# Kernel tuning notes

Measured on AMD Instinct MI355X. Metric: run time of the kernel, lower is better.

The kernel has to match this reference:

```python
import jax, jax.numpy as jnp
import numpy as np

MAX_WORDS = 256  # = batch['labels'].shape[1]


def _align(hidden, word_ids, max_words):
    """Batched segment-mean: (B,S,D) subtoken states -> (B,max_words,D) word states.
    Equivalent to align_subtokens_to_words applied per sample (word_ids all valid)."""
    B, S, D = hidden.shape
    seg = (word_ids.astype(jnp.int32) + jnp.arange(B, dtype=jnp.int32)[:, None] * max_words).reshape(-1)
    sums = jax.ops.segment_sum(hidden.reshape(-1, D), seg, num_segments=B * max_words)
    cnts = jax.ops.segment_sum(jnp.ones((B * S,), hidden.dtype), seg, num_segments=B * max_words)
    out = jnp.where(cnts[:, None] > 0, sums / jnp.maximum(cnts, 1.0)[:, None], 0.0)
    return out.reshape(B, max_words, D)


def setup_inputs() -> dict:
    key = jax.random.key(0)
    ks = jax.random.split(key, 8)
    B, S, D, W = 64, 512, 768, MAX_WORDS
    h_hing_sub = jax.random.normal(ks[0], (B, S, D), dtype=jnp.float32)
    h_rob_sub = jax.random.normal(ks[1], (B, S, D), dtype=jnp.float32)
    hing_word_ids = jnp.sort(jax.random.randint(ks[2], (B, S), 0, W), axis=-1).astype(jnp.int32)
    rob_word_ids = jnp.sort(jax.random.randint(ks[3], (B, S), 0, W), axis=-1).astype(jnp.int32)
    num_words = jax.random.randint(ks[4], (B,), 1, W).astype(jnp.int32)
    router_w1 = jax.random.normal(ks[5], (2 * D, 256), dtype=jnp.float32) * (1.0 / np.sqrt(2 * D))
    router_b1 = jnp.zeros((256,), jnp.float32)
    router_w2 = jax.random.normal(ks[6], (256, 1), dtype=jnp.float32) * (1.0 / 16.0)
    router_b2 = jnp.zeros((1,), jnp.float32)
    head_w = jax.random.normal(ks[7], (D, 7), dtype=jnp.float32) * (1.0 / np.sqrt(D))
    head_b = jnp.zeros((7,), jnp.float32)
    return {
        'h_hing_sub': h_hing_sub, 'h_rob_sub': h_rob_sub,
        'hing_word_ids': hing_word_ids, 'rob_word_ids': rob_word_ids,
        'num_words': num_words,
        'router_w1': router_w1, 'router_b1': router_b1,
        'router_w2': router_w2, 'router_b2': router_b2,
        'head_w': head_w, 'head_b': head_b,
    }


def reference(h_hing_sub, h_rob_sub, hing_word_ids, rob_word_ids, num_words,
              router_w1, router_b1, router_w2, router_b2, head_w, head_b):
    W = MAX_WORDS
    # scatter-mean subtokens -> words (the dominant custom-kernel op)
    h_hing = _align(h_hing_sub, hing_word_ids, W)   # (B, W, 768)
    h_rob = _align(h_rob_sub, rob_word_ids, W)      # (B, W, 768)
    # token-level MLP router on concatenated word states (router_input='both')
    router_in = jnp.concatenate([h_hing, h_rob], axis=-1)             # (B, W, 1536)
    hdn = jax.nn.relu(jnp.einsum('bwd,dh->bwh', router_in, router_w1) + router_b1)
    alpha = jax.nn.sigmoid(jnp.einsum('bwh,ho->bwo', hdn, router_w2) + router_b2)  # (B, W, 1)
    blended = alpha * h_hing + (1.0 - alpha) * h_rob                  # (B, W, 768)
    logits = jnp.einsum('bwd,dl->bwl', blended, head_w) + head_b      # (B, W, num_labels)
    l2_disagreement = jnp.linalg.norm(h_hing - h_rob, axis=-1)        # (B, W)
    return logits, alpha.squeeze(-1), l2_disagreement
```

## Files before the change

### kernel.cpp

```cpp
#include <hip/hip_runtime.h>
#include <hip/hip_bf16.h>
#include <math.h>

#define BATCH 64
#define SEQ   512
#define DIM   768
#define NW    256
#define NT    (BATCH * NW)
#define KDIM  1536
#define HID   256
#define NL    7

#define BM  32
#define BK  64
#define BKP 72
#define NKT (KDIM / BK)

typedef __bf16 bf16_t;
typedef bf16_t bf16x4 __attribute__((ext_vector_type(4)));
typedef bf16_t bf16x8 __attribute__((ext_vector_type(8)));
typedef float  f32x4  __attribute__((ext_vector_type(4)));

__global__ __launch_bounds__(256) void prep_kernel(
    const float* __restrict__ w1, bf16_t* __restrict__ w1t,
    const int* __restrict__ idh, const int* __restrict__ idr,
    int* __restrict__ starts)
{
    if (blockIdx.x < 192) {
        int kc = blockIdx.x >> 3;
        int kg = blockIdx.x & 7;
        int n  = threadIdx.x;
        bf16x8 v;
        #pragma unroll
        for (int j = 0; j < 8; j++)
            v[j] = (bf16_t)w1[(size_t)(kc * 64 + kg * 8 + j) * HID + n];
        *(bf16x8*)(w1t + (size_t)kc * (HID * BK) + n * BK + kg * 8) = v;
    } else {
        int blk = blockIdx.x - 192;
        int t = blk >> 6;
        int b = blk & 63;
        const int* ids = (t ? idr : idh) + b * SEQ;
        int w = threadIdx.x;
        int lo = 0, hi = SEQ;
        while (lo < hi) {
            int m = (lo + hi) >> 1;
            if (ids[m] < w) lo = m + 1; else hi = m;
        }
        int* row = starts + blk * 257;
        row[w] = lo;
        if (w == 0) row[256] = SEQ;
    }
}

__global__ __launch_bounds__(256) void align_kernel(
    const float* __restrict__ hh, const float* __restrict__ hr,
    const int* __restrict__ starts, bf16_t* __restrict__ X)
{
    int bid  = blockIdx.x;
    int swz  = (bid & 7) * 3072 + (bid >> 3);

    int idx  = swz * 256 + threadIdx.x;
    int rest = idx / 192;
    int c    = idx - rest * 192;
    rest     = __builtin_amdgcn_readfirstlane(rest);
    int w    = rest & 255;
    int t    = (rest >> 8) & 1;
    int b    = rest >> 9;

    const int* st = starts + (t * 64 + b) * 257;
    int lo = st[w];
    int hi = st[w + 1];

    const f32x4* src = (const f32x4*)((t ? hr : hh) + (size_t)b * SEQ * DIM);
    bf16_t*      dst = X + (size_t)b * NW * KDIM + (size_t)w * KDIM
                         + t * DIM + c * 4;

    bf16x4 o = {};
    int n = hi - lo;
    if (n > 0) {
        f32x4 acc = src[(size_t)lo * 192 + c];
        for (int s = lo + 1; s < hi; s++) {
            f32x4 v = src[(size_t)s * 192 + c];
            acc[0] += v[0]; acc[1] += v[1];
            acc[2] += v[2]; acc[3] += v[3];
        }
        float inv = 1.0f / (float)n;
        o[0] = (bf16_t)(acc[0] * inv);
        o[1] = (bf16_t)(acc[1] * inv);
        o[2] = (bf16_t)(acc[2] * inv);
        o[3] = (bf16_t)(acc[3] * inv);
    }
    *(bf16x4*)dst = o;
}

__global__ __launch_bounds__(256) void gemm_alpha_kernel(
    const bf16_t* __restrict__ X, const bf16_t* __restrict__ w1t,
    const float* __restrict__ b1, const float* __restrict__ w2,
    const float* __restrict__ b2, float* __restrict__ out)
{
    __shared__ __align__(16) bf16_t Xs[BM][BKP];
    __shared__ __align__(16) bf16_t Ws[HID][BKP];
    __shared__ float alpha_acc[BM];

    int tid   = threadIdx.x;
    int lane  = tid & 63;
    int wv    = tid >> 6;
    int row16 = lane & 15;
    int quad  = lane >> 4;
    int tok0  = blockIdx.x * BM;

    f32x4 acc[2][4];
    #pragma unroll
    for (int mi = 0; mi < 2; mi++)
        #pragma unroll
        for (int ni = 0; ni < 4; ni++)
            acc[mi][ni] = (f32x4){0.f, 0.f, 0.f, 0.f};

    int xr = tid >> 3;
    int xc = tid & 7;

    for (int kc = 0; kc < NKT; kc++) {
        {
            const uint4* src = (const uint4*)(X + (size_t)(tok0 + xr) * KDIM + kc * BK + xc * 8);
            *(uint4*)(&Xs[xr][xc * 8]) = *src;
        }
        {
            const uint4* srcb = (const uint4*)(w1t + (size_t)kc * (HID * BK));
            #pragma unroll
            for (int i = 0; i < 8; i++) {
                int cidx = tid + i * 256;
                *(uint4*)(&Ws[cidx >> 3][(cidx & 7) * 8]) = srcb[cidx];
            }
        }
        __syncthreads();
        #pragma unroll
        for (int kk2 = 0; kk2 < 2; kk2++) {
            bf16x8 af[2], bfg[4];
            #pragma unroll
            for (int mi = 0; mi < 2; mi++)
                af[mi] = *(const bf16x8*)(&Xs[mi * 16 + row16][kk2 * 32 + quad * 8]);
            #pragma unroll
            for (int ni = 0; ni < 4; ni++)
                bfg[ni] = *(const bf16x8*)(&Ws[wv * 64 + ni * 16 + row16][kk2 * 32 + quad * 8]);
            #pragma unroll
            for (int mi = 0; mi < 2; mi++)
                #pragma unroll
                for (int ni = 0; ni < 4; ni++)
                    acc[mi][ni] = __builtin_amdgcn_mfma_f32_16x16x32_bf16(
                        af[mi], bfg[ni], acc[mi][ni], 0, 0, 0);
        }
        __syncthreads();
    }

    float w2v[4], b1v[4];
    #pragma unroll
    for (int ni = 0; ni < 4; ni++) {
        int col = wv * 64 + ni * 16 + row16;
        w2v[ni] = w2[col];
        b1v[ni] = b1[col];
    }
    if (tid < BM) alpha_acc[tid] = 0.f;
    __syncthreads();

    #pragma unroll
    for (int mi = 0; mi < 2; mi++) {
        #pragma unroll
        for (int r = 0; r < 4; r++) {
            float p = 0.f;
            #pragma unroll
            for (int ni = 0; ni < 4; ni++) {
                float v = acc[mi][ni][r] + b1v[ni];
                v = v > 0.f ? v : 0.f;
                p += v * w2v[ni];
            }
            p += __shfl_xor(p, 1);
            p += __shfl_xor(p, 2);
            p += __shfl_xor(p, 4);
            p += __shfl_xor(p, 8);
            if (row16 == 0)
                atomicAdd(&alpha_acc[mi * 16 + quad * 4 + r], p);
        }
    }
    __syncthreads();
    if (tid < BM) {
        float a = 1.f / (1.f + expf(-(alpha_acc[tid] + b2[0])));
        out[(size_t)NT * NL + tok0 + tid] = a;
    }
}

__global__ __launch_bounds__(256) void blend_kernel(
    const bf16_t* __restrict__ X, const float* __restrict__ hw,
    const float* __restrict__ hb, float* __restrict__ out)
{
    __shared__ float hws[NL * DIM];
    int tid  = threadIdx.x;
    int lane = tid & 63;
    int wv   = tid >> 6;

    for (int i = tid; i < DIM * NL; i += 256) {
        int d = i / NL, l = i - d * NL;
        hws[l * DIM + d] = hw[i];
    }
    __syncthreads();

    int g   = lane >> 3;
    int u   = lane & 7;
    int tok = blockIdx.x * 32 + wv * 8 + g;

    float a = out[(size_t)NT * NL + tok];
    const bf16_t* xrow = X + (size_t)tok * KDIM;

    float lg[NL] = {0.f, 0.f, 0.f, 0.f, 0.f, 0.f, 0.f};
    float l2 = 0.f;

    #pragma unroll
    for (int k = 0; k < 12; k++) {
        int d0 = (k * 8 + u) * 8;
        bf16x8 hp = *(const bf16x8*)(xrow + d0);
        bf16x8 rp = *(const bf16x8*)(xrow + DIM + d0);
        float bl[8];
        #pragma unroll
        for (int e = 0; e < 8; e++) {
            float hhv = (float)hp[e];
            float hrv = (float)rp[e];
            float df  = hhv - hrv;
            bl[e] = fmaf(a, df, hrv);
            l2 = fmaf(df, df, l2);
        }
        #pragma unroll
        for (int l = 0; l < NL; l++) {
            f32x4 wA = *(const f32x4*)(&hws[l * DIM + d0]);
            f32x4 wB = *(const f32x4*)(&hws[l * DIM + d0 + 4]);
            lg[l] += bl[0]*wA[0] + bl[1]*wA[1] + bl[2]*wA[2] + bl[3]*wA[3]
                   + bl[4]*wB[0] + bl[5]*wB[1] + bl[6]*wB[2] + bl[7]*wB[3];
        }
    }

    #pragma unroll
    for (int off = 1; off < 8; off <<= 1) {
        #pragma unroll
        for (int l = 0; l < NL; l++) lg[l] += __shfl_xor(lg[l], off);
        l2 += __shfl_xor(l2, off);
    }

    if (u < NL) {
        float v = (u == 0) ? lg[0] : (u == 1) ? lg[1] : (u == 2) ? lg[2]
                : (u == 3) ? lg[3] : (u == 4) ? lg[4] : (u == 5) ? lg[5] : lg[6];
        out[(size_t)tok * NL + u] = v + hb[u];
    } else {
        out[(size_t)NT * NL + NT + tok] = sqrtf(l2);
    }
}

extern "C" void kernel_launch(void* const* d_in, const int* in_sizes, int n_in,
                              void* d_out, int out_size, void* d_ws, size_t ws_size,
                              hipStream_t stream)
{
    const float* hh  = (const float*)d_in[0];
    const float* hr  = (const float*)d_in[1];
    const int*   idh = (const int*)d_in[2];
    const int*   idr = (const int*)d_in[3];
    const float* w1  = (const float*)d_in[5];
    const float* b1  = (const float*)d_in[6];
    const float* w2  = (const float*)d_in[7];
    const float* b2  = (const float*)d_in[8];
    const float* hw  = (const float*)d_in[9];
    const float* hb  = (const float*)d_in[10];
    float* out = (float*)d_out;

    bf16_t* X      = (bf16_t*)d_ws;
    bf16_t* w1t    = X + (size_t)NT * KDIM;
    int*    starts = (int*)(w1t + (size_t)NKT * HID * BK);

    prep_kernel<<<320, 256, 0, stream>>>(w1, w1t, idh, idr, starts);
    align_kernel<<<24576, 256, 0, stream>>>(hh, hr, starts, X);
    gemm_alpha_kernel<<<NT / BM, 256, 0, stream>>>(X, w1t, b1, w2, b2, out);
    blend_kernel<<<512, 256, 0, stream>>>(X, hw, hb, out);
}
```

Baseline: 281.0 us.

## Fuse blend/logits/L2 into router GEMM kernel and unroll align accumulation

Merges the blend kernel into the GEMM+alpha kernel. Each block computes alpha for its 32 tokens, keeps it in shared memory, reuses the Ws shared buffer to hold the head weights, then computes logits and L2 for the same tokens. This removes a kernel launch and the global round-trip of alpha. X rows are re-read while likely still in cache. The align loop now uses two independent accumulators, which adds memory-level parallelism. The costs are a serial tail stage in the GEMM kernel, a reload of the head weights per block (512 blocks, same as before), and a changed summation order.

```diff
diff --git a/kernel.cpp b/kernel.cpp
--- a/kernel.cpp
+++ b/kernel.cpp
@@ -78,29 +78,39 @@
     bf16x4 o = {};
     int n = hi - lo;
     if (n > 0) {
-        f32x4 acc = src[(size_t)lo * 192 + c];
-        for (int s = lo + 1; s < hi; s++) {
-            f32x4 v = src[(size_t)s * 192 + c];
-            acc[0] += v[0]; acc[1] += v[1];
-            acc[2] += v[2]; acc[3] += v[3];
-        }
+        f32x4 acc0 = {0.f, 0.f, 0.f, 0.f};
+        f32x4 acc1 = {0.f, 0.f, 0.f, 0.f};
+        int s = lo;
+        for (; s + 2 <= hi; s += 2) {
+            f32x4 v0 = src[(size_t)s * 192 + c];
+            f32x4 v1 = src[(size_t)(s + 1) * 192 + c];
+            acc0 += v0;
+            acc1 += v1;
+        }
+        if (s < hi)
+            acc0 += src[(size_t)s * 192 + c];
+        acc0 += acc1;
         float inv = 1.0f / (float)n;
-        o[0] = (bf16_t)(acc[0] * inv);
-        o[1] = (bf16_t)(acc[1] * inv);
-        o[2] = (bf16_t)(acc[2] * inv);
-        o[3] = (bf16_t)(acc[3] * inv);
+        o[0] = (bf16_t)(acc0[0] * inv);
+        o[1] = (bf16_t)(acc0[1] * inv);
+        o[2] = (bf16_t)(acc0[2] * inv);
+        o[3] = (bf16_t)(acc0[3] * inv);
     }
     *(bf16x4*)dst = o;
 }
 
-__global__ __launch_bounds__(256) void gemm_alpha_kernel(
+__global__ __launch_bounds__(256) void gemm_blend_kernel(
     const bf16_t* __restrict__ X, const bf16_t* __restrict__ w1t,
     const float* __restrict__ b1, const float* __restrict__ w2,
-    const float* __restrict__ b2, float* __restrict__ out)
-{
-    __shared__ __align__(16) bf16_t Xs[BM][BKP];
-    __shared__ __align__(16) bf16_t Ws[HID][BKP];
+    const float* __restrict__ b2, const float* __restrict__ hw,
+    const float* __restrict__ hb, float* __restrict__ out)
+{
+    __shared__ __align__(16) unsigned char smem[4608 + 36864];
+    bf16_t (*Xs)[BKP] = (bf16_t (*)[BKP])smem;
+    bf16_t (*Ws)[BKP] = (bf16_t (*)[BKP])(smem + 4608);
+    float*  hws       = (float*)(smem + 4608);
     __shared__ float alpha_acc[BM];
+    __shared__ float alpha_s[BM];
 
     int tid   = threadIdx.x;
     int lane  = tid & 63;
@@ -181,21 +191,6 @@
                 atomicAdd(&alpha_acc[mi * 16 + quad * 4 + r], p);
         }
     }
-    __syncthreads();
-    if (tid < BM) {
-        float a = 1.f / (1.f + expf(-(alpha_acc[tid] + b2[0])));
-        out[(size_t)NT * NL + tok0 + tid] = a;
-    }
-}
-
-__global__ __launch_bounds__(256) void blend_kernel(
-    const bf16_t* __restrict__ X, const float* __restrict__ hw,
-    const float* __restrict__ hb, float* __restrict__ out)
-{
-    __shared__ float hws[NL * DIM];
-    int tid  = threadIdx.x;
-    int lane = tid & 63;
-    int wv   = tid >> 6;
 
     for (int i = tid; i < DIM * NL; i += 256) {
         int d = i / NL, l = i - d * NL;
@@ -203,52 +198,61 @@
     }
     __syncthreads();
 
-    int g   = lane >> 3;
-    int u   = lane & 7;
-    int tok = blockIdx.x * 32 + wv * 8 + g;
-
-    float a = out[(size_t)NT * NL + tok];
-    const bf16_t* xrow = X + (size_t)tok * KDIM;
-
-    float lg[NL] = {0.f, 0.f, 0.f, 0.f, 0.f, 0.f, 0.f};
-    float l2 = 0.f;
-
-    #pragma unroll
-    for (int k = 0; k < 12; k++) {
-        int d0 = (k * 8 + u) * 8;
-        bf16x8 hp = *(const bf16x8*)(xrow + d0);
-        bf16x8 rp = *(const bf16x8*)(xrow + DIM + d0);
-        float bl[8];
-        #pragma unroll
-        for (int e = 0; e < 8; e++) {
-            float hhv = (float)hp[e];
-            float hrv = (float)rp[e];
-            float df  = hhv - hrv;
-            bl[e] = fmaf(a, df, hrv);
-            l2 = fmaf(df, df, l2);
-        }
-        #pragma unroll
-        for (int l = 0; l < NL; l++) {
-            f32x4 wA = *(const f32x4*)(&hws[l * DIM + d0]);
-            f32x4 wB = *(const f32x4*)(&hws[l * DIM + d0 + 4]);
-            lg[l] += bl[0]*wA[0] + bl[1]*wA[1] + bl[2]*wA[2] + bl[3]*wA[3]
-                   + bl[4]*wB[0] + bl[5]*wB[1] + bl[6]*wB[2] + bl[7]*wB[3];
-        }
-    }
-
-    #pragma unroll
-    for (int off = 1; off < 8; off <<= 1) {
-        #pragma unroll
-        for (int l = 0; l < NL; l++) lg[l] += __shfl_xor(lg[l], off);
-        l2 += __shfl_xor(l2, off);
-    }
-
-    if (u < NL) {
-        float v = (u == 0) ? lg[0] : (u == 1) ? lg[1] : (u == 2) ? lg[2]
-                : (u == 3) ? lg[3] : (u == 4) ? lg[4] : (u == 5) ? lg[5] : lg[6];
-        out[(size_t)tok * NL + u] = v + hb[u];
-    } else {
-        out[(size_t)NT * NL + NT + tok] = sqrtf(l2);
+    if (tid < BM) {
+        float a = 1.f / (1.f + expf(-(alpha_acc[tid] + b2[0])));
+        alpha_s[tid] = a;
+        out[(size_t)NT * NL + tok0 + tid] = a;
+    }
+    __syncthreads();
+
+    {
+        int g   = lane >> 3;
+        int u   = lane & 7;
+        int tl  = wv * 8 + g;
+        int tok = tok0 + tl;
+        float a = alpha_s[tl];
+        const bf16_t* xrow = X + (size_t)tok * KDIM;
+
+        float lg[NL] = {0.f, 0.f, 0.f, 0.f, 0.f, 0.f, 0.f};
+        float l2 = 0.f;
+
+        #pragma unroll
+        for (int k = 0; k < 12; k++) {
+            int d0 = (k * 8 + u) * 8;
+            bf16x8 hp = *(const bf16x8*)(xrow + d0);
+            bf16x8 rp = *(const bf16x8*)(xrow + DIM + d0);
+            float bl[8];
+            #pragma unroll
+            for (int e = 0; e < 8; e++) {
+                float hhv = (float)hp[e];
+                float hrv = (float)rp[e];
+                float df  = hhv - hrv;
+                bl[e] = fmaf(a, df, hrv);
+                l2 = fmaf(df, df, l2);
+            }
+            #pragma unroll
+            for (int l = 0; l < NL; l++) {
+                f32x4 wA = *(const f32x4*)(&hws[l * DIM + d0]);
+                f32x4 wB = *(const f32x4*)(&hws[l * DIM + d0 + 4]);
+                lg[l] += bl[0]*wA[0] + bl[1]*wA[1] + bl[2]*wA[2] + bl[3]*wA[3]
+                       + bl[4]*wB[0] + bl[5]*wB[1] + bl[6]*wB[2] + bl[7]*wB[3];
+            }
+        }
+
+        #pragma unroll
+        for (int off = 1; off < 8; off <<= 1) {
+            #pragma unroll
+            for (int l = 0; l < NL; l++) lg[l] += __shfl_xor(lg[l], off);
+            l2 += __shfl_xor(l2, off);
+        }
+
+        if (u < NL) {
+            float v = (u == 0) ? lg[0] : (u == 1) ? lg[1] : (u == 2) ? lg[2]
+                    : (u == 3) ? lg[3] : (u == 4) ? lg[4] : (u == 5) ? lg[5] : lg[6];
+            out[(size_t)tok * NL + u] = v + hb[u];
+        } else {
+            out[(size_t)NT * NL + NT + tok] = sqrtf(l2);
+        }
     }
 }
 
@@ -274,6 +278,6 @@
 
     prep_kernel<<<320, 256, 0, stream>>>(w1, w1t, idh, idr, starts);
     align_kernel<<<24576, 256, 0, stream>>>(hh, hr, starts, X);
-    gemm_alpha_kernel<<<NT / BM, 256, 0, stream>>>(X, w1t, b1, w2, b2, out);
-    blend_kernel<<<512, 256, 0, stream>>>(X, hw, hb, out);
-}
+    gemm_blend_kernel<<<NT / BM, 256, 0, stream>>>(X, w1t, b1, w2, b2,
+                                                   hw, hb, out);
+}
```

Result: no change. 275.6 us (-1.9%).
